# Optimization experiments

Hardware: AMD Instinct MI355X
Metric: run time of the kernel (lower is better)

Reference implementation:

```python
import jax, jax.numpy as jnp
import numpy as np

N_BLOCKS = 16
N_FEATS = 64
SCALE = 2
RGB_RANGE = 255.0
RGB_MEAN = np.array([0.4488, 0.4371, 0.4040], dtype=np.float32)  # DIV2K mean used by EDSR MeanShift


def conv2d(x, w, b=None):
    # x: [N,C,H,W], w: [O,I,kh,kw], SAME padding, stride 1
    y = jax.lax.conv_general_dilated(x, w, (1, 1), 'SAME',
                                     dimension_numbers=('NCHW', 'OIHW', 'NCHW'))
    if b is not None:
        y = y + b[None, :, None, None]
    return y


def ste_sign(x):
    # sign with straight-through estimator (identity gradient)
    return x + jax.lax.stop_gradient(jnp.sign(x) - x)


def bin_conv(x, w):
    # XNOR-style 1-bit conv: binarize activations to {-1,+1} (sign, STE),
    # binarize weights to sign(w) * alpha where alpha = per-output-channel mean(|w|).
    xb = ste_sign(x)
    alpha = jnp.mean(jnp.abs(w), axis=(1, 2, 3), keepdims=True)  # [O,1,1,1]
    wb = ste_sign(w) * alpha
    return conv2d(xb, wb)


def pixel_shuffle(x, r):
    # torch nn.PixelShuffle semantics
    n, c, h, w = x.shape
    x = x.reshape(n, c // (r * r), r, r, h, w)
    x = x.transpose(0, 1, 4, 2, 5, 3)  # [n, c', h, r, w, r]
    return x.reshape(n, c // (r * r), h * r, w * r)


def setup_inputs() -> dict:
    key = jax.random.key(0)
    ks = jax.random.split(key, 8)
    fan = 1.0 / np.sqrt(N_FEATS * 9)
    x = jax.random.uniform(ks[0], (16, 3, 128, 128), jnp.float32) * RGB_RANGE
    w_head = jax.random.normal(ks[1], (N_FEATS, 3, 3, 3), jnp.float32) * (1.0 / np.sqrt(3 * 9))
    w_body = jax.random.normal(ks[2], (N_BLOCKS, 2, N_FEATS, N_FEATS, 3, 3), jnp.float32) * fan
    w_body_last = jax.random.normal(ks[3], (N_FEATS, N_FEATS, 3, 3), jnp.float32) * fan
    w_up = jax.random.normal(ks[4], (N_FEATS * SCALE * SCALE, N_FEATS, 3, 3), jnp.float32) * fan
    w_tail = jax.random.normal(ks[5], (3, N_FEATS, 3, 3), jnp.float32) * fan
    b_tail = jnp.zeros((3,), jnp.float32)
    return {'x': x, 'w_head': w_head, 'w_body': w_body, 'w_body_last': w_body_last,
            'w_up': w_up, 'w_tail': w_tail, 'b_tail': b_tail}


def reference(x, w_head, w_body, w_body_last, w_up, w_tail, b_tail):
    shift = jnp.asarray(RGB_RANGE * RGB_MEAN).reshape(1, 3, 1, 1)
    x = x - shift                      # sub_mean
    h = conv2d(x, w_head)              # full-precision head, [N,64,H,W]
    r = h
    for i in range(N_BLOCKS):          # fixed layer count
        t = bin_conv(r, w_body[i, 0])
        t = jnp.tanh(t)
        t = bin_conv(t, w_body[i, 1])
        r = r + t                      # res_scale = 1
    r = bin_conv(r, w_body_last)
    res = r + h                        # global skip; this is `out`
    t = conv2d(res, w_up)              # 64 -> 64*r^2
    t = pixel_shuffle(t, SCALE)        # [N,64,H*r,W*r]
    t = conv2d(t, w_tail, b_tail)      # 64 -> 3
    out_img = t + shift                # add_mean
    return (out_img, res)
```

## Files before the change

kernel.cpp:

```cpp
#include <hip/hip_runtime.h>
#include <stdint.h>

typedef unsigned long long u64;
typedef unsigned int u32;
using i32x4  = __attribute__((ext_vector_type(4))) int;
using i32x16 = __attribute__((ext_vector_type(16))) int;
using f32x4  = __attribute__((ext_vector_type(4))) float;

#define HW 16384

#define OFF_R      0ull
#define OFF_SGR    67108864ull
#define OFF_SGT    69206016ull
#define OFF_NZT    71303168ull
#define OFF_WBSG   73400320ull
#define OFF_ALPHA  74616832ull
#define OFF_WEFF   74625280ull

__global__ __launch_bounds__(256) void k_prep_wbsg(const float* __restrict__ wbody, const float* __restrict__ wlast,
                                                   signed char* __restrict__ wB, float* __restrict__ alpha){
  int t = blockIdx.x*256 + threadIdx.x;
  if (t >= 33*9*64) return;
  int o = t & 63, tap = (t>>6)%9, cid = t/(64*9);
  const float* src = (cid < 32) ? (wbody + (size_t)cid*36864) : wlast;
  u32 d[16];
  #pragma unroll
  for (int c4=0;c4<16;c4++){
    u32 v=0;
    #pragma unroll
    for (int j=0;j<4;j++){
      float w = src[(o*64 + c4*4+j)*9 + tap];
      v |= ((w < 0.f) ? 0xFFu : 0x01u) << (8*j);
    }
    d[c4]=v;
  }
  i32x4* dst = (i32x4*)(wB + ((size_t)(cid*9+tap)*64 + o)*64);
  #pragma unroll
  for (int k=0;k<4;k++){ i32x4 v; v[0]=(int)d[4*k]; v[1]=(int)d[4*k+1]; v[2]=(int)d[4*k+2]; v[3]=(int)d[4*k+3]; dst[k]=v; }
  if (tap==0){
    float s=0.f;
    for (int ci=0;ci<64;ci++)
      #pragma unroll
      for (int tp=0;tp<9;tp++) s += fabsf(src[(o*64+ci)*9+tp]);
    alpha[cid*64+o] = s * (1.0f/576.0f);
  }
}

__global__ __launch_bounds__(256) void k_prep_weff(const float* __restrict__ wup, const float* __restrict__ wtail,
                                                   float* __restrict__ weff){
  int idx = blockIdx.x*256 + threadIdx.x;
  int rx = idx & 3;
  int px = (idx >> 2) & 1;
  int base = idx >> 3;
  int o  = base % 3;
  int t2 = base / 3;
  int ci = t2 & 63;
  int ry = (t2 >> 6) & 3;
  int py = (t2 >> 8) & 1;
  int e  = t2 >> 9;
  int ex = e % 3, ey = e / 3;
  int ry_off = (py - 2) + ry;
  int rx_off = (px - 2) + rx;
  float acc = 0.f;
  for (int dy=0; dy<3; dy++){
    if (ey==1 && dy==0) continue;
    if (ey==2 && dy==2) continue;
    int pydy = py + dy - 1;
    int sy = ((pydy + 4) >> 1) - 2;
    int vy = (pydy + 4) & 1;
    int a = ry_off + 1 - sy;
    if (a < 0 || a > 2) continue;
    for (int dx=0; dx<3; dx++){
      if (ex==0 && dx==0) continue;
      if (ex==2 && dx==2) continue;
      int pxdx = px + dx - 1;
      int sx = ((pxdx + 4) >> 1) - 2;
      int vx = (pxdx + 4) & 1;
      int b = rx_off + 1 - sx;
      if (b < 0 || b > 2) continue;
      for (int c=0; c<64; c++){
        int u = c*4 + vy*2 + vx;
        acc += wtail[((o*64+c)*3+dy)*3+dx] * wup[((u*64+ci)*3+a)*3+b];
      }
    }
  }
  weff[idx] = acc;
}

__global__ __launch_bounds__(256) void k_head(const float* __restrict__ x, const float* __restrict__ wh,
                                              float* __restrict__ r, float* __restrict__ h, u64* __restrict__ sgR){
  __shared__ float wl[64*27];
  for (int j=threadIdx.x; j<64*27; j+=256) wl[j] = wh[j];
  __syncthreads();
  const int id = blockIdx.x*256 + threadIdx.x;
  const int n = id >> 14, p = id & 16383;
  const int yy = p >> 7, xx = p & 127;
  float xv[27];
  const float sh[3] = {114.444f, 111.4605f, 103.02f};
  #pragma unroll
  for (int tap=0; tap<9; tap++){
    int Yq = yy + tap/3 - 1, Xq = xx + tap%3 - 1;
    bool v = ((unsigned)Yq < 128u) && ((unsigned)Xq < 128u);
    int q = (Yq << 7) + Xq;
    #pragma unroll
    for (int c=0; c<3; c++)
      xv[c*9+tap] = v ? (x[(size_t)(n*3+c)*HW + q] - sh[c]) : 0.f;
  }
  u64 sg = 0;
  for (int o=0; o<64; o++){
    float acc = 0.f;
    #pragma unroll
    for (int j=0; j<27; j++) acc += wl[o*27+j] * xv[j];
    r[(size_t)(n*64+o)*HW + p] = acc;
    h[(size_t)(n*64+o)*HW + p] = acc;
    sg |= (u64)(acc < 0.f) << o;
  }
  sgR[id] = sg;
}

template<int MODE>
__global__ __launch_bounds__(256) void k_bconv(const u64* __restrict__ sgIn, const u64* __restrict__ nzIn,
                                               const signed char* __restrict__ wB, const float* __restrict__ alphaC,
                                               float* __restrict__ rbuf, u64* __restrict__ sgOut,
                                               u64* __restrict__ nzOut, float* __restrict__ resbuf){
  __shared__ signed char Abytes[4*68*80];

  const int bx = blockIdx.x;
  const int n  = bx >> 7;
  const int rem = bx & 127;
  const int y0 = (rem >> 1) << 1;
  const int x0 = (rem & 1) << 6;

  const int lane = threadIdx.x & 63;
  const int wid  = threadIdx.x >> 6;
  const int rrow = wid >> 1;
  const int och  = wid & 1;
  const int nn   = lane & 31;
  const int q    = lane >> 5;

  i32x4 Bf[9][2];
  #pragma unroll
  for (int t=0;t<9;t++)
    #pragma unroll
    for (int h=0;h<2;h++)
      Bf[t][h] = *(const i32x4*)(wB + ((size_t)(t*64 + och*32 + nn))*64 + h*32 + q*16);

  for (int s = threadIdx.x; s < 4*66; s += 256){
    int g = s/66, c = s%66;
    int y = y0 + g - 1, xcol = x0 + c - 1;
    u64 pos=0, neg=0;
    if (((unsigned)y < 128u) && ((unsigned)xcol < 128u)){
      int p = (n<<14) + (y<<7) + xcol;
      u64 sg = sgIn[p];
      if (MODE==1){ u64 nz = nzIn[p]; pos = nz & ~sg; neg = nz & sg; }
      else        { pos = ~sg;        neg = sg; }
    }
    u32 plo=(u32)pos, phi=(u32)(pos>>32), nlo=(u32)neg, nhi=(u32)(neg>>32);
    u32 tmp[16];
    #pragma unroll
    for (int i=0;i<16;i++){
      u32 np = ((i<8) ? (plo >> (4*i)) : (phi >> (4*i-32))) & 0xFu;
      u32 nm = ((i<8) ? (nlo >> (4*i)) : (nhi >> (4*i-32))) & 0xFu;
      u32 bp = (np * 0x00204081u) & 0x01010101u;
      u32 bn = (nm * 0x00204081u) & 0x01010101u;
      tmp[i] = bp | (bn * 0xFFu);
    }
    i32x4* dst = (i32x4*)&Abytes[(g*68 + c)*80];
    #pragma unroll
    for (int k=0;k<4;k++){ i32x4 v; v[0]=(int)tmp[4*k]; v[1]=(int)tmp[4*k+1]; v[2]=(int)tmp[4*k+2]; v[3]=(int)tmp[4*k+3]; dst[k]=v; }
  }
  __syncthreads();

  const float al = (MODE==0) ? 0.f : alphaC[och*32 + nn];

  for (int xh=0; xh<2; xh++){
    i32x16 acc;
    #pragma unroll
    for (int k=0;k<16;k++) acc[k]=0;

    const i32x4* Ap = (const i32x4*)&Abytes[(rrow*68 + xh*32 + nn)*80 + q*16];
    #pragma unroll
    for (int dy=0;dy<3;dy++)
      #pragma unroll
      for (int dx=0;dx<3;dx++){
        const int t = dy*3+dx;
        #pragma unroll
        for (int h=0;h<2;h++){
          i32x4 a = Ap[(dy*68+dx)*5 + h*2];
          acc = __builtin_amdgcn_mfma_i32_32x32x32_i8(a, Bf[t][h], acc, 0, 0, 0);
        }
      }

    const int ybase = y0 + rrow, xbase = x0 + xh*32;

    if (MODE==0){
      u32 sgc=0, nzc=0;
      #pragma unroll
      for (int reg=0; reg<16; reg++){
        u64 bs = __ballot(acc[reg] < 0);
        u64 bn = __ballot(acc[reg] != 0);
        const int px0 = (reg&3) + ((reg>>2)<<3);
        sgc = (lane==px0  ) ? (u32)bs       : sgc;
        sgc = (lane==px0+4) ? (u32)(bs>>32) : sgc;
        nzc = (lane==px0  ) ? (u32)bn       : nzc;
        nzc = (lane==px0+4) ? (u32)(bn>>32) : nzc;
      }
      if (lane < 32){
        int p = (n<<14) + (ybase<<7) + xbase + lane;
        ((u32*)sgOut)[p*2 + och] = sgc;
        ((u32*)nzOut)[p*2 + och] = nzc;
      }
    } else if (MODE==1){
      float newr[16];
      float* rp = rbuf + ((size_t)((n<<6) + och*32 + nn))*HW + (ybase<<7) + xbase;
      #pragma unroll
      for (int k2=0;k2<4;k2++){
        f32x4 rv = *(f32x4*)(rp + 4*q + 8*k2);
        #pragma unroll
        for (int j=0;j<4;j++){ rv[j] += al * (float)acc[4*k2+j]; newr[4*k2+j] = rv[j]; }
        *(f32x4*)(rp + 4*q + 8*k2) = rv;
      }
      u32 sgc=0;
      #pragma unroll
      for (int reg=0; reg<16; reg++){
        u64 b = __ballot(newr[reg] < 0.f);
        const int px0 = (reg&3) + ((reg>>2)<<3);
        sgc = (lane==px0  ) ? (u32)b       : sgc;
        sgc = (lane==px0+4) ? (u32)(b>>32) : sgc;
      }
      if (lane < 32){
        int p = (n<<14) + (ybase<<7) + xbase + lane;
        ((u32*)sgOut)[p*2 + och] = sgc;
      }
    } else {
      float* hp = resbuf + ((size_t)((n<<6) + och*32 + nn))*HW + (ybase<<7) + xbase;
      #pragma unroll
      for (int k2=0;k2<4;k2++){
        f32x4 hv = *(f32x4*)(hp + 4*q + 8*k2);
        #pragma unroll
        for (int j=0;j<4;j++) hv[j] += al * (float)acc[4*k2+j];
        *(f32x4*)(hp + 4*q + 8*k2) = hv;
      }
    }
  }
}

__global__ __launch_bounds__(128) void k_tail(const float* __restrict__ res, const float* __restrict__ weff,
                                              const float* __restrict__ btail, float* __restrict__ out){
  const int x = threadIdx.x;
  const int Y = blockIdx.x;
  const int n = blockIdx.y;
  const int py = Y & 1, y = Y >> 1;
  const int ey = (Y==0) ? 1 : ((Y==255) ? 2 : 0);
  const float* Ws = weff + (size_t)(((ey*3+1)*2+py)) * 6144;
  float acc[3][2] = {{0.f,0.f},{0.f,0.f},{0.f,0.f}};
  for (int ry=0; ry<4; ry++){
    const int yy = y + (py-2) + ry;
    const bool rowv = ((unsigned)yy < 128u);
    const float* Wr = Ws + ry*1536;
    const float* rp = res + (size_t)n*64*HW + yy*128 + x;
    for (int ci=0; ci<64; ci++){
      const float* pp = rp + (size_t)ci*HW;
      float v[5];
      #pragma unroll
      for (int j=0; j<5; j++){
        int xxc = x - 2 + j;
        v[j] = (rowv && (unsigned)xxc < 128u) ? pp[j-2] : 0.f;
      }
      const float* Wc = Wr + ci*24;
      #pragma unroll
      for (int o=0; o<3; o++)
        #pragma unroll
        for (int px=0; px<2; px++)
          #pragma unroll
          for (int rx=0; rx<4; rx++)
            acc[o][px] += Wc[(o*2+px)*4+rx] * v[px+rx];
    }
  }
  const float sh[3] = {114.444f, 111.4605f, 103.02f};
  #pragma unroll
  for (int o=0; o<3; o++){
    #pragma unroll
    for (int px=0; px<2; px++){
      int X = 2*x + px;
      if (X == 0 || X == 255) continue;
      out[(size_t)((n*3+o)*256+Y)*256 + X] = acc[o][px] + btail[o] + sh[o];
    }
  }
}

__global__ __launch_bounds__(256) void k_border(const float* __restrict__ res, const float* __restrict__ weff,
                                                const float* __restrict__ btail, float* __restrict__ out){
  int t = blockIdx.x*256 + threadIdx.x;
  if (t >= 8192) return;
  int side = t & 1;
  int Y = (t >> 1) & 255;
  int n = t >> 9;
  int X = side ? 255 : 0;
  int px = side, x = side ? 127 : 0;
  int py = Y & 1, y = Y >> 1;
  int ey = (Y==0) ? 1 : ((Y==255) ? 2 : 0);
  int ex = side ? 2 : 0;
  const float* Ws = weff + (size_t)((ey*3+ex)*2+py) * 6144;
  float acc[3] = {0.f,0.f,0.f};
  for (int ry=0; ry<4; ry++){
    int yy = y + (py-2) + ry;
    bool rowv = ((unsigned)yy < 128u);
    const float* rp = res + (size_t)n*64*HW + yy*128;
    for (int ci=0; ci<64; ci++){
      const float* Wc = Ws + ry*1536 + ci*24 + px*4;
      #pragma unroll
      for (int rx=0; rx<4; rx++){
        int xxc = x + (px-2) + rx;
        float v = (rowv && (unsigned)xxc < 128u) ? rp[(size_t)ci*HW + xxc] : 0.f;
        acc[0] += Wc[0*8+rx] * v;
        acc[1] += Wc[1*8+rx] * v;
        acc[2] += Wc[2*8+rx] * v;
      }
    }
  }
  const float sh[3] = {114.444f, 111.4605f, 103.02f};
  for (int o=0; o<3; o++)
    out[(size_t)((n*3+o)*256+Y)*256 + X] = acc[o] + btail[o] + sh[o];
}

extern "C" void kernel_launch(void* const* d_in, const int* in_sizes, int n_in,
                              void* d_out, int out_size, void* d_ws, size_t ws_size,
                              hipStream_t stream) {
  const float* x      = (const float*)d_in[0];
  const float* w_head = (const float*)d_in[1];
  const float* w_body = (const float*)d_in[2];
  const float* w_last = (const float*)d_in[3];
  const float* w_up   = (const float*)d_in[4];
  const float* w_tail = (const float*)d_in[5];
  const float* b_tail = (const float*)d_in[6];

  char* ws = (char*)d_ws;
  float* r     = (float*)(ws + OFF_R);
  u64*  sgR    = (u64*) (ws + OFF_SGR);
  u64*  sgT    = (u64*) (ws + OFF_SGT);
  u64*  nzT    = (u64*) (ws + OFF_NZT);
  signed char* wBsg = (signed char*)(ws + OFF_WBSG);
  float* alpha = (float*)(ws + OFF_ALPHA);
  float* weff  = (float*)(ws + OFF_WEFF);

  float* out = (float*)d_out;
  float* res = out + 3145728;

  k_prep_wbsg<<<75, 256, 0, stream>>>(w_body, w_last, wBsg, alpha);
  k_prep_weff<<<432, 256, 0, stream>>>(w_up, w_tail, weff);
  k_head<<<1024, 256, 0, stream>>>(x, w_head, r, res, sgR);
  for (int i=0; i<16; i++){
    k_bconv<0><<<2048, 256, 0, stream>>>(sgR, nullptr, wBsg + (size_t)(2*i)*36864,
                                         nullptr, nullptr, sgT, nzT, nullptr);
    k_bconv<1><<<2048, 256, 0, stream>>>(sgT, nzT, wBsg + (size_t)(2*i+1)*36864,
                                         alpha + (2*i+1)*64, r, sgR, nullptr, nullptr);
  }
  k_bconv<2><<<2048, 256, 0, stream>>>(sgR, nullptr, wBsg + (size_t)32*36864,
                                       alpha + 32*64, nullptr, nullptr, nullptr, res);
  k_tail<<<dim3(256,16), 128, 0, stream>>>(res, weff, b_tail, out);
  k_border<<<32, 256, 0, stream>>>(res, weff, b_tail, out);
}
```

Baseline: 1.353 ms.

## Fuse residual-block loop into persistent cooperative kernel with register-resident residual

Replaces the 32 per-layer binary-conv launches with one cooperative persistent kernel of 512 blocks, each owning four image rows. Each block keeps the float residual in registers across all 16 blocks, so it no longer reads and writes it through global memory every layer. Both convolutions of a block run back to back through rolling shared-memory row rings, recomputing halo rows of the intermediate activation locally. Only the packed sign bits pass through global memory, with a software grid barrier between residual blocks. The cost is about 1.5x redundant work on the first convolution, barrier latency, and a dependence on all 512 blocks being co-resident; if the cooperative launch fails, the old per-layer path runs instead.

```diff
diff --git a/kernel.cpp b/kernel.cpp
--- a/kernel.cpp
+++ b/kernel.cpp
@@ -10,8 +10,8 @@
 #define HW 16384
 
 #define OFF_R      0ull
-#define OFF_SGR    67108864ull
-#define OFF_SGT    69206016ull
+#define OFF_SG0    67108864ull
+#define OFF_SG1    69206016ull
 #define OFF_NZT    71303168ull
 #define OFF_WBSG   73400320ull
 #define OFF_ALPHA  74616832ull
@@ -118,6 +118,191 @@
   sgR[id] = sg;
 }
 
+__device__ __forceinline__ void bconv_tile(const char* ring, int so0, int so1, int so2,
+                                           int c0bytes, const signed char* wb, int nn, int q,
+                                           i32x16& a0, i32x16& a1){
+  int soff[3] = {so0, so1, so2};
+  #pragma unroll
+  for (int dy=0; dy<3; dy++){
+    const char* rbase = ring + soff[dy] + c0bytes + nn*80 + q*16;
+    #pragma unroll
+    for (int dx=0; dx<3; dx++){
+      const char* ab = rbase + dx*80;
+      const char* wbt = (const char*)wb + (size_t)((dy*3+dx)*64 + nn)*64 + q*16;
+      #pragma unroll
+      for (int hh=0; hh<2; hh++){
+        i32x4 a  = *(const i32x4*)(ab + hh*32);
+        i32x4 b0 = *(const i32x4*)(wbt + hh*32);
+        i32x4 b1 = *(const i32x4*)(wbt + 2048 + hh*32);
+        a0 = __builtin_amdgcn_mfma_i32_32x32x32_i8(a, b0, a0, 0, 0, 0);
+        a1 = __builtin_amdgcn_mfma_i32_32x32x32_i8(a, b1, a1, 0, 0, 0);
+      }
+    }
+  }
+}
+
+__device__ __forceinline__ void upd_row(float (&rrow)[2][16], const i32x16& a0, const i32x16& a1,
+                                        float al0, float al1, float* nv0, float* nv1){
+  #pragma unroll
+  for (int t=0; t<16; t++){
+    rrow[0][t] += al0 * (float)a0[t]; nv0[t] = rrow[0][t];
+    rrow[1][t] += al1 * (float)a1[t]; nv1[t] = rrow[1][t];
+  }
+}
+
+__device__ __forceinline__ void gridbar(int* cnt, int* sns, int nb, int sense, int tid){
+  __syncthreads();
+  if (tid == 0){
+    __threadfence();
+    int prev = __hip_atomic_fetch_add(cnt, 1, __ATOMIC_ACQ_REL, __HIP_MEMORY_SCOPE_AGENT);
+    if (prev == nb - 1){
+      __hip_atomic_store(cnt, 0, __ATOMIC_RELAXED, __HIP_MEMORY_SCOPE_AGENT);
+      __hip_atomic_store(sns, sense, __ATOMIC_RELEASE, __HIP_MEMORY_SCOPE_AGENT);
+    } else {
+      while (__hip_atomic_load(sns, __ATOMIC_ACQUIRE, __HIP_MEMORY_SCOPE_AGENT) < sense)
+        __builtin_amdgcn_s_sleep(8);
+    }
+    __threadfence();
+  }
+  __syncthreads();
+}
+
+__global__ __launch_bounds__(256, 2) void k_persist(const float* __restrict__ rglob,
+                                                    u64* __restrict__ sgA, u64* __restrict__ sgB,
+                                                    const signed char* __restrict__ wBsg,
+                                                    const float* __restrict__ alpha,
+                                                    int* __restrict__ bar){
+  __shared__ alignas(16) char smem[62880];
+  char* sgRg = smem;
+  char* tRg  = smem + 31680;
+
+  const int tid  = threadIdx.x;
+  const int b    = blockIdx.x;
+  const int n    = b >> 5;
+  const int y0   = (b & 31) << 2;
+  const int lane = tid & 63;
+  const int wid  = tid >> 6;
+  const int nn   = lane & 31;
+  const int q    = lane >> 5;
+
+  float rreg[4][2][16];
+  #pragma unroll
+  for (int rr=0; rr<4; rr++)
+    #pragma unroll
+    for (int och=0; och<2; och++)
+      #pragma unroll
+      for (int k2=0; k2<4; k2++){
+        f32x4 v = *(const f32x4*)(rglob + (size_t)(n*64 + och*32 + nn)*HW + (y0+rr)*128 + wid*32 + q*4 + k2*8);
+        #pragma unroll
+        for (int j=0; j<4; j++) rreg[rr][och][k2*4+j] = v[j];
+      }
+
+  int sense = 0;
+  for (int i=0; i<16; i++){
+    const u64* inb = (i & 1) ? sgB : sgA;
+    u64* outb      = (i & 1) ? sgA : sgB;
+    const signed char* wb1 = wBsg + (size_t)(2*i)*36864;
+    const signed char* wb2 = wb1 + 36864;
+    const float al0 = alpha[(2*i+1)*64 + nn];
+    const float al1 = alpha[(2*i+1)*64 + 32 + nn];
+
+    for (int k=0; k<8; k++){
+      {
+        int ry = y0 - 2 + k;
+        int slotD = (ry + 6) % 3;
+        for (int c = tid; c < 132; c += 256){
+          u64 neg = 0, pos = 0;
+          int ic = c - 2;
+          if (((unsigned)ry < 128u) && ((unsigned)ic < 128u)){
+            u64 sg = inb[(n<<14) + (ry<<7) + ic];
+            neg = sg; pos = ~sg;
+          }
+          u32 plo=(u32)pos, phi=(u32)(pos>>32), nlo=(u32)neg, nhi=(u32)(neg>>32);
+          u32 tmp[16];
+          #pragma unroll
+          for (int t2=0; t2<16; t2++){
+            u32 np = ((t2<8) ? (plo >> (4*t2)) : (phi >> (4*t2-32))) & 0xFu;
+            u32 nm = ((t2<8) ? (nlo >> (4*t2)) : (nhi >> (4*t2-32))) & 0xFu;
+            u32 bp = (np * 0x00204081u) & 0x01010101u;
+            u32 bn = (nm * 0x00204081u) & 0x01010101u;
+            tmp[t2] = bp | (bn * 0xFFu);
+          }
+          i32x4* dst = (i32x4*)(sgRg + slotD*10560 + c*80);
+          #pragma unroll
+          for (int kk=0; kk<4; kk++){
+            i32x4 v; v[0]=(int)tmp[4*kk]; v[1]=(int)tmp[4*kk+1]; v[2]=(int)tmp[4*kk+2]; v[3]=(int)tmp[4*kk+3];
+            dst[kk] = v;
+          }
+        }
+      }
+      __syncthreads();
+
+      if (k >= 2){
+        int ty = y0 - 3 + k;
+        int slotT = (ty + 6) % 3;
+        char* tslot = tRg + slotT*10400;
+        if ((unsigned)ty >= 128u){
+          for (int idx = tid; idx < 2600; idx += 256) ((u32*)tslot)[idx] = 0;
+        } else {
+          if (tid < 8){
+            int col = (tid < 4) ? 0 : 129;
+            ((i32x4*)(tslot + col*80))[tid & 3] = (i32x4){0,0,0,0};
+          }
+          i32x16 a0, a1;
+          #pragma unroll
+          for (int t=0; t<16; t++){ a0[t]=0; a1[t]=0; }
+          bconv_tile(sgRg, ((ty-1+6)%3)*10560, ((ty+6)%3)*10560, ((ty+1+6)%3)*10560,
+                     (32*wid + 1)*80, wb1, nn, q, a0, a1);
+          #pragma unroll
+          for (int reg=0; reg<16; reg++){
+            int tc = 32*wid + (reg&3) + ((reg>>2)<<3) + 4*q;
+            char* p = tslot + (tc+1)*80 + nn;
+            int v0 = a0[reg], v1 = a1[reg];
+            p[0]  = (signed char)((v0>0) - (v0<0));
+            p[32] = (signed char)((v1>0) - (v1<0));
+          }
+        }
+      }
+      __syncthreads();
+
+      if (k >= 4){
+        int cy = y0 - 4 + k;
+        i32x16 a0, a1;
+        #pragma unroll
+        for (int t=0; t<16; t++){ a0[t]=0; a1[t]=0; }
+        bconv_tile(tRg, ((cy-1+6)%3)*10400, ((cy+6)%3)*10400, ((cy+1+6)%3)*10400,
+                   (32*wid)*80, wb2, nn, q, a0, a1);
+        float nv0[16], nv1[16];
+        switch (k){
+          case 4: upd_row(rreg[0], a0, a1, al0, al1, nv0, nv1); break;
+          case 5: upd_row(rreg[1], a0, a1, al0, al1, nv0, nv1); break;
+          case 6: upd_row(rreg[2], a0, a1, al0, al1, nv0, nv1); break;
+          default: upd_row(rreg[3], a0, a1, al0, al1, nv0, nv1); break;
+        }
+        u32 s0 = 0, s1 = 0;
+        #pragma unroll
+        for (int reg=0; reg<16; reg++){
+          int px0 = (reg&3) + ((reg>>2)<<3);
+          u64 b0 = __ballot(nv0[reg] < 0.f);
+          u64 b1 = __ballot(nv1[reg] < 0.f);
+          s0 = (lane==px0  ) ? (u32)b0       : s0;
+          s0 = (lane==px0+4) ? (u32)(b0>>32) : s0;
+          s1 = (lane==px0  ) ? (u32)b1       : s1;
+          s1 = (lane==px0+4) ? (u32)(b1>>32) : s1;
+        }
+        if (lane < 32){
+          int p = (n<<14) + (cy<<7) + (wid<<5) + lane;
+          ((u32*)outb)[p*2]     = s0;
+          ((u32*)outb)[p*2 + 1] = s1;
+        }
+      }
+      __syncthreads();
+    }
+    sense++;
+    gridbar(bar, bar+1, (int)gridDim.x, sense, tid);
+  }
+}
+
 template<int MODE>
 __global__ __launch_bounds__(256) void k_bconv(const u64* __restrict__ sgIn, const u64* __restrict__ nzIn,
                                                const signed char* __restrict__ wB, const float* __restrict__ alphaC,
@@ -337,26 +522,34 @@
 
   char* ws = (char*)d_ws;
   float* r     = (float*)(ws + OFF_R);
-  u64*  sgR    = (u64*) (ws + OFF_SGR);
-  u64*  sgT    = (u64*) (ws + OFF_SGT);
+  u64*  sg0    = (u64*) (ws + OFF_SG0);
+  u64*  sg1    = (u64*) (ws + OFF_SG1);
   u64*  nzT    = (u64*) (ws + OFF_NZT);
   signed char* wBsg = (signed char*)(ws + OFF_WBSG);
   float* alpha = (float*)(ws + OFF_ALPHA);
   float* weff  = (float*)(ws + OFF_WEFF);
+  int*   bar   = (int*)  (ws + OFF_NZT);
 
   float* out = (float*)d_out;
   float* res = out + 3145728;
 
   k_prep_wbsg<<<75, 256, 0, stream>>>(w_body, w_last, wBsg, alpha);
   k_prep_weff<<<432, 256, 0, stream>>>(w_up, w_tail, weff);
-  k_head<<<1024, 256, 0, stream>>>(x, w_head, r, res, sgR);
-  for (int i=0; i<16; i++){
-    k_bconv<0><<<2048, 256, 0, stream>>>(sgR, nullptr, wBsg + (size_t)(2*i)*36864,
-                                         nullptr, nullptr, sgT, nzT, nullptr);
-    k_bconv<1><<<2048, 256, 0, stream>>>(sgT, nzT, wBsg + (size_t)(2*i+1)*36864,
-                                         alpha + (2*i+1)*64, r, sgR, nullptr, nullptr);
-  }
-  k_bconv<2><<<2048, 256, 0, stream>>>(sgR, nullptr, wBsg + (size_t)32*36864,
+  k_head<<<1024, 256, 0, stream>>>(x, w_head, r, res, sg0);
+
+  hipMemsetAsync((void*)bar, 0, 64, stream);
+  const float* rc = r;
+  void* args[6] = {(void*)&rc, (void*)&sg0, (void*)&sg1, (void*)&wBsg, (void*)&alpha, (void*)&bar};
+  hipError_t e = hipLaunchCooperativeKernel((void*)k_persist, dim3(512), dim3(256), args, 0, stream);
+  if (e != hipSuccess){
+    for (int i=0; i<16; i++){
+      k_bconv<0><<<2048, 256, 0, stream>>>(sg0, nullptr, wBsg + (size_t)(2*i)*36864,
+                                           nullptr, nullptr, sg1, nzT, nullptr);
+      k_bconv<1><<<2048, 256, 0, stream>>>(sg1, nzT, wBsg + (size_t)(2*i+1)*36864,
+                                           alpha + (2*i+1)*64, r, sg0, nullptr, nullptr);
+    }
+  }
+  k_bconv<2><<<2048, 256, 0, stream>>>(sg0, nullptr, wBsg + (size_t)32*36864,
                                        alpha + 32*64, nullptr, nullptr, nullptr, res);
   k_tail<<<dim3(256,16), 128, 0, stream>>>(res, weff, b_tail, out);
   k_border<<<32, 256, 0, stream>>>(res, weff, b_tail, out);
```

After: 4.995 ms. 269% more time.

## Store residual stream in fp16 and remap tail blocks per XCD

Applied to the files above, without the earlier changes.

The residual buffer r, updated in place by every second binary conv, is stored as fp16 instead of fp32, halving its read/write traffic across the 16 residual blocks. Sign bits are computed from the rounded fp16 value so they stay consistent with what is stored. Separately, the tail kernel's grid is flattened and remapped so consecutive block IDs (spread across XCDs) map each XCD to two batch images, improving L2 locality. The fp16 residual adds rounding error to the accumulated stream, which can flip signs that feed later binarizations.

```diff
diff --git a/kernel.cpp b/kernel.cpp
--- a/kernel.cpp
+++ b/kernel.cpp
@@ -3,15 +3,17 @@
 
 typedef unsigned long long u64;
 typedef unsigned int u32;
+typedef _Float16 f16;
 using i32x4  = __attribute__((ext_vector_type(4))) int;
 using i32x16 = __attribute__((ext_vector_type(16))) int;
 using f32x4  = __attribute__((ext_vector_type(4))) float;
+using f16x4  = __attribute__((ext_vector_type(4))) _Float16;
 
 #define HW 16384
 
 #define OFF_R      0ull
-#define OFF_SGR    67108864ull
-#define OFF_SGT    69206016ull
+#define OFF_SG0    67108864ull
+#define OFF_SG1    69206016ull
 #define OFF_NZT    71303168ull
 #define OFF_WBSG   73400320ull
 #define OFF_ALPHA  74616832ull
@@ -88,7 +90,7 @@
 }
 
 __global__ __launch_bounds__(256) void k_head(const float* __restrict__ x, const float* __restrict__ wh,
-                                              float* __restrict__ r, float* __restrict__ h, u64* __restrict__ sgR){
+                                              f16* __restrict__ r, float* __restrict__ h, u64* __restrict__ sgR){
   __shared__ float wl[64*27];
   for (int j=threadIdx.x; j<64*27; j+=256) wl[j] = wh[j];
   __syncthreads();
@@ -111,9 +113,10 @@
     float acc = 0.f;
     #pragma unroll
     for (int j=0; j<27; j++) acc += wl[o*27+j] * xv[j];
-    r[(size_t)(n*64+o)*HW + p] = acc;
+    f16 rv = (f16)acc;
+    r[(size_t)(n*64+o)*HW + p] = rv;
     h[(size_t)(n*64+o)*HW + p] = acc;
-    sg |= (u64)(acc < 0.f) << o;
+    sg |= (u64)((float)rv < 0.f) << o;
   }
   sgR[id] = sg;
 }
@@ -121,7 +124,7 @@
 template<int MODE>
 __global__ __launch_bounds__(256) void k_bconv(const u64* __restrict__ sgIn, const u64* __restrict__ nzIn,
                                                const signed char* __restrict__ wB, const float* __restrict__ alphaC,
-                                               float* __restrict__ rbuf, u64* __restrict__ sgOut,
+                                               f16* __restrict__ rbuf, u64* __restrict__ sgOut,
                                                u64* __restrict__ nzOut, float* __restrict__ resbuf){
   __shared__ signed char Abytes[4*68*80];
 
@@ -212,13 +215,17 @@
       }
     } else if (MODE==1){
       float newr[16];
-      float* rp = rbuf + ((size_t)((n<<6) + och*32 + nn))*HW + (ybase<<7) + xbase;
+      f16* rp = rbuf + ((size_t)((n<<6) + och*32 + nn))*HW + (ybase<<7) + xbase;
       #pragma unroll
       for (int k2=0;k2<4;k2++){
-        f32x4 rv = *(f32x4*)(rp + 4*q + 8*k2);
+        f16x4 rv4 = *(f16x4*)(rp + 4*q + 8*k2);
         #pragma unroll
-        for (int j=0;j<4;j++){ rv[j] += al * (float)acc[4*k2+j]; newr[4*k2+j] = rv[j]; }
-        *(f32x4*)(rp + 4*q + 8*k2) = rv;
+        for (int j=0;j<4;j++){
+          float rv = (float)rv4[j] + al * (float)acc[4*k2+j];
+          rv4[j] = (f16)rv;
+          newr[4*k2+j] = (float)rv4[j];
+        }
+        *(f16x4*)(rp + 4*q + 8*k2) = rv4;
       }
       u32 sgc=0;
       #pragma unroll
@@ -247,9 +254,12 @@
 
 __global__ __launch_bounds__(128) void k_tail(const float* __restrict__ res, const float* __restrict__ weff,
                                               const float* __restrict__ btail, float* __restrict__ out){
+  const int id = blockIdx.x;
+  const int xcd = id & 7;
+  const int l = id >> 3;
+  const int n = xcd*2 + (l & 1);
+  const int Y = l >> 1;
   const int x = threadIdx.x;
-  const int Y = blockIdx.x;
-  const int n = blockIdx.y;
   const int py = Y & 1, y = Y >> 1;
   const int ey = (Y==0) ? 1 : ((Y==255) ? 2 : 0);
   const float* Ws = weff + (size_t)(((ey*3+1)*2+py)) * 6144;
@@ -336,9 +346,9 @@
   const float* b_tail = (const float*)d_in[6];
 
   char* ws = (char*)d_ws;
-  float* r     = (float*)(ws + OFF_R);
-  u64*  sgR    = (u64*) (ws + OFF_SGR);
-  u64*  sgT    = (u64*) (ws + OFF_SGT);
+  f16*  r      = (f16*) (ws + OFF_R);
+  u64*  sg0    = (u64*) (ws + OFF_SG0);
+  u64*  sg1    = (u64*) (ws + OFF_SG1);
   u64*  nzT    = (u64*) (ws + OFF_NZT);
   signed char* wBsg = (signed char*)(ws + OFF_WBSG);
   float* alpha = (float*)(ws + OFF_ALPHA);
@@ -349,15 +359,15 @@
 
   k_prep_wbsg<<<75, 256, 0, stream>>>(w_body, w_last, wBsg, alpha);
   k_prep_weff<<<432, 256, 0, stream>>>(w_up, w_tail, weff);
-  k_head<<<1024, 256, 0, stream>>>(x, w_head, r, res, sgR);
+  k_head<<<1024, 256, 0, stream>>>(x, w_head, r, res, sg0);
   for (int i=0; i<16; i++){
-    k_bconv<0><<<2048, 256, 0, stream>>>(sgR, nullptr, wBsg + (size_t)(2*i)*36864,
-                                         nullptr, nullptr, sgT, nzT, nullptr);
-    k_bconv<1><<<2048, 256, 0, stream>>>(sgT, nzT, wBsg + (size_t)(2*i+1)*36864,
-                                         alpha + (2*i+1)*64, r, sgR, nullptr, nullptr);
-  }
-  k_bconv<2><<<2048, 256, 0, stream>>>(sgR, nullptr, wBsg + (size_t)32*36864,
+    k_bconv<0><<<2048, 256, 0, stream>>>(sg0, nullptr, wBsg + (size_t)(2*i)*36864,
+                                         nullptr, nullptr, sg1, nzT, nullptr);
+    k_bconv<1><<<2048, 256, 0, stream>>>(sg1, nzT, wBsg + (size_t)(2*i+1)*36864,
+                                         alpha + (2*i+1)*64, r, sg0, nullptr, nullptr);
+  }
+  k_bconv<2><<<2048, 256, 0, stream>>>(sg0, nullptr, wBsg + (size_t)32*36864,
                                        alpha + 32*64, nullptr, nullptr, nullptr, res);
-  k_tail<<<dim3(256,16), 128, 0, stream>>>(res, weff, b_tail, out);
+  k_tail<<<4096, 128, 0, stream>>>(res, weff, b_tail, out);
   k_border<<<32, 256, 0, stream>>>(res, weff, b_tail, out);
 }
```

Measured after the change: 1.290 ms. -4.7%, faster.
